# Kernel optimization log

Measured on AMD Instinct MI355X. Metric: run time of the kernel, lower is better.

The kernel has to match this reference:

```python
import jax, jax.numpy as jnp
import numpy as np

L, B, D, H = 4096, 4, 1024, 16
HD = D // H
SCALAR = 700.0


def setup_inputs() -> dict:
    key = jax.random.key(0)
    ks = jax.random.split(key, 9)
    bound = np.sqrt(6.0 / (D + D)).astype(np.float32)  # xavier_uniform for square weights
    def xavier(k):
        return jax.random.uniform(k, (D, D), jnp.float32, -bound, bound)
    return {
        "input_tensor": jax.random.normal(ks[0], (L, B, D), jnp.float32),
        "num_heads": H,
        "Wq": xavier(ks[1]), "bq": jnp.zeros((D,), jnp.float32),
        "Wk": xavier(ks[2]), "bk": jnp.zeros((D,), jnp.float32),
        "Wv": xavier(ks[3]), "bv": jnp.zeros((D,), jnp.float32),
        "Wo": xavier(ks[4]), "bo": jnp.zeros((D,), jnp.float32),
        "scalar": jnp.asarray(SCALAR, jnp.float32),
    }


def reference(input_tensor, num_heads, Wq, bq, Wk, bk, Wv, bv, Wo, bo, scalar):
    l, b, d = input_tensor.shape
    h = num_heads
    hd = d // h
    scaling = hd ** -0.5
    X = jnp.transpose(input_tensor, (1, 0, 2))  # (b, l, d)
    q = (X @ Wq.T + bq) * scaling
    k = X @ Wk.T + bk
    v = X @ Wv.T + bv
    # split heads: (b, l, h*hd) -> (b, h, l, hd)
    q = q.reshape(b, l, h, hd).transpose(0, 2, 1, 3)
    k = k.reshape(b, l, h, hd).transpose(0, 2, 1, 3)
    v = v.reshape(b, l, h, hd).transpose(0, 2, 1, 3)
    # linear attention: (K^T V) then Q @ (...)  -> O(l * hd^2)
    kv = jnp.einsum('bhld,bhle->bhde', k, v)        # (b, h, hd, hd)
    out = jnp.einsum('bhld,bhde->bhle', q, kv) / scalar  # (b, h, l, hd)
    # faithful to einops '(b h) l d -> b l (d h)': feature layout is (hd, h)
    out = out.transpose(0, 2, 3, 1).reshape(b, l, d)  # (b, l, hd*h)
    out = out @ Wo.T + bo
    return jnp.transpose(out, (1, 0, 2))  # (l, b, d)
```

## Files before the change

kernel.cpp:

```cpp
#include <hip/hip_runtime.h>
#include <stdint.h>
#include <stddef.h>

typedef unsigned short ushort_t;
typedef __attribute__((ext_vector_type(8))) short short8;
typedef __attribute__((ext_vector_type(4))) float f32x4;
typedef __attribute__((ext_vector_type(4))) float float4v;

#define L_DIM 4096
#define B_DIM 4
#define D_DIM 1024
#define H_DIM 16
#define HD_DIM 64
#define M_DIM (L_DIM * B_DIM)

__device__ __forceinline__ float bf2f(ushort_t u) {
    union { unsigned int i; float f; } v; v.i = ((unsigned int)u) << 16; return v.f;
}
__device__ __forceinline__ ushort_t f2bf(float f) {
    union { float f; unsigned int i; } v; v.f = f;
    unsigned int r = v.i + 0x7FFFu + ((v.i >> 16) & 1u);
    return (ushort_t)(r >> 16);
}
__device__ __forceinline__ unsigned int pk2(float a, float b) {
    return (unsigned int)f2bf(a) | ((unsigned int)f2bf(b) << 16);
}
__device__ __forceinline__ void gload16(const ushort_t* g, ushort_t* l) {
    __builtin_amdgcn_global_load_lds(
        (const __attribute__((address_space(1))) unsigned int*)g,
        (__attribute__((address_space(3))) unsigned int*)l, 16, 0, 0);
}

union U32x4S8 { unsigned int u[4]; short8 s; };
__device__ __forceinline__ short8 read_frag66(const ushort_t* p) {
    U32x4S8 r;
    r.u[0] = *(const unsigned int*)(p + 0);
    r.u[1] = *(const unsigned int*)(p + 2);
    r.u[2] = *(const unsigned int*)(p + 4);
    r.u[3] = *(const unsigned int*)(p + 6);
    return r.s;
}

__global__ void detect_kernel(const ushort_t* __restrict__ scal, int* __restrict__ flag)
{
    *flag = (scal[0] == 0) ? 1 : 0;
}

__global__ void convert_b_kernel(const void* bq, const void* bk, const void* bv,
                                 const void* bo, float* __restrict__ bias_f,
                                 const int* __restrict__ flag)
{
    int fl = *flag;
    int idx = blockIdx.x * 256 + threadIdx.x;
    int j = idx >> 10, i = idx & 1023;
    const void* p = (j == 0) ? bq : (j == 1) ? bk : (j == 2) ? bv : bo;
    bias_f[idx] = fl ? ((const float*)p)[i] : bf2f(((const ushort_t*)p)[i]);
}

__global__ void convert_w_kernel(const void* Wk, const void* Wv, const void* Wo,
                                 const void* Wq,
                                 ushort_t* __restrict__ Wkc, ushort_t* __restrict__ Wvc,
                                 ushort_t* __restrict__ Wpc, ushort_t* __restrict__ Wqc,
                                 const int* __restrict__ flag)
{
    int fl = *flag;
    int z = blockIdx.z;
    int idx = blockIdx.x * 256 + threadIdx.x;
    const void* src = (z == 0) ? Wk : (z == 1) ? Wv : (z == 2) ? Wo : Wq;
    ushort_t* dst   = (z == 0) ? Wkc : (z == 1) ? Wvc : (z == 2) ? Wpc : Wqc;
    size_t sidx;
    if (z != 2) sidx = (size_t)idx;
    else {
        int n = idx >> 10, f = idx & 1023;
        int hh = f >> 6, e = f & 63;
        sidx = (size_t)n * D_DIM + e * H_DIM + hh;
    }
    dst[idx] = fl ? f2bf(((const float*)src)[sidx]) : ((const ushort_t*)src)[sidx];
}

__global__ void convert_x_kernel(const void* __restrict__ X, ushort_t* __restrict__ Xb,
                                 const int* __restrict__ flag)
{
    int fl = *flag;
    size_t i8 = ((size_t)blockIdx.x * 256 + threadIdx.x) * 8;
    if (fl) {
        const float4v* p = (const float4v*)((const float*)X + i8);
        float4v f0 = p[0], f1 = p[1];
        uint4 u;
        u.x = pk2(f0.x, f0.y); u.y = pk2(f0.z, f0.w);
        u.z = pk2(f1.x, f1.y); u.w = pk2(f1.z, f1.w);
        *(uint4*)(Xb + i8) = u;
    } else {
        *(uint4*)(Xb + i8) = *(const uint4*)((const ushort_t*)X + i8);
    }
}

#define BARRIER() asm volatile("s_barrier" ::: "memory")
#define VMWAIT(N) asm volatile("s_waitcnt vmcnt(" #N ")" ::: "memory")

#define STAGE_A(q, kt, dbuf) {                                                 \
    int kc_ = (kt) < 16 ? (kt) : 15;                                           \
    int row_ = ((w & 4) << 5) + (q) * 32 + ((w & 3) << 3) + lrow8;             \
    gload16(A + (size_t)(a_base + (m0 + row_) * astride) * D_DIM               \
                + kc_ * 64 + kcol,                                             \
            sA + (dbuf) * 16384 + row_ * 64 + lcol8); }

#define STAGE_B(o, kt, dbuf) {                                                 \
    int kc_ = (kt) < 16 ? (kt) : 15;                                           \
    int nr_ = (o) * 64 + (w << 3) + lrow8;                                     \
    gload16(W + (size_t)(n0 + nr_) * D_DIM + kc_ * 64 + kcol,                  \
            sB + (dbuf) * 16384 + nr_ * 64 + lcol8); }

#define PROJ_PHASE(S, STAGE0, STAGE1, WAITSTMT)                                \
  {                                                                            \
    short8 af[2][2];                                                           \
    _Pragma("unroll")                                                          \
    for (int j = 0; j < 2; ++j)                                                \
      _Pragma("unroll")                                                        \
      for (int ks = 0; ks < 2; ++ks)                                           \
        af[j][ks] = *(const short8*)&lAc[(awbase + ((S) * 2 + j) * 16) * 64    \
                                         + ((ks * 32 + q8) ^ swz)];            \
    STAGE0; STAGE1;                                                            \
    BARRIER();                                                                 \
    __builtin_amdgcn_s_setprio(1);                                             \
    _Pragma("unroll")                                                          \
    for (int j = 0; j < 2; ++j)                                                \
      _Pragma("unroll")                                                        \
      for (int nt = 0; nt < 4; ++nt)                                           \
        _Pragma("unroll")                                                      \
        for (int ks = 0; ks < 2; ++ks)                                         \
          acc[(S) * 2 + j][nt] = __builtin_amdgcn_mfma_f32_16x16x32_bf16(      \
              af[j][ks], bf[nt][ks], acc[(S) * 2 + j][nt], 0, 0, 0);           \
    __builtin_amdgcn_s_setprio(0);                                             \
    WAITSTMT;                                                                  \
    BARRIER();                                                                 \
  }

__global__ __launch_bounds__(512) void proj_kernel(
    const ushort_t* __restrict__ A, int a_base0, int a_zstride, int astride,
    const ushort_t* __restrict__ W0, int w_z,
    const float* __restrict__ bias0, int b_z,
    void* __restrict__ out, int o_base0, int o_zstride, int ostride,
    const int* __restrict__ flag, int o_dyn)
{
    extern __shared__ ushort_t smem[];
    ushort_t* sA = smem;
    ushort_t* sB = smem + 32768;

    const int z      = blockIdx.z;
    const int a_base = a_base0 + z * a_zstride;
    const int o_base = o_base0 + z * o_zstride;
    const ushort_t* W = W0 + (size_t)z * w_z * (D_DIM * D_DIM);
    const float* bias = bias0 + z * b_z * D_DIM;
    const int ofl  = o_dyn & *flag;
    const int t    = threadIdx.x;
    const int m0   = blockIdx.x * 256;
    const int n0   = blockIdx.y * 256;
    const int w    = t >> 6;
    const int lane = t & 63;
    const int quad = lane >> 4;
    const int l16  = lane & 15;
    const int wm   = w >> 2;
    const int wn   = w & 3;

    const int lrow8 = lane >> 3;
    const int lcol8 = (lane & 7) * 8;
    const int kcol  = (((lane & 7) ^ lrow8) << 3);

    const int awbase = wm * 128 + l16;
    const int bnbase = wn * 64 + l16;
    const int q8     = quad * 8;
    const int swz    = (l16 & 7) << 3;

    f32x4 acc[8][4];
#pragma unroll
    for (int i = 0; i < 8; i++)
#pragma unroll
        for (int j = 0; j < 4; j++) acc[i][j] = f32x4{0.f, 0.f, 0.f, 0.f};

    STAGE_B(0, 0, 0) STAGE_B(1, 0, 0) STAGE_B(2, 0, 0) STAGE_B(3, 0, 0)
    STAGE_A(0, 0, 0) STAGE_A(1, 0, 0) STAGE_A(2, 0, 0) STAGE_A(3, 0, 0)
    STAGE_B(0, 1, 1) STAGE_B(1, 1, 1)
    VMWAIT(4);
    BARRIER();

    for (int c = 0; c < 16; ++c) {
        const int buf = c & 1, nbuf = buf ^ 1;
        const ushort_t* lAc = sA + buf * 16384;
        const ushort_t* lBc = sB + buf * 16384;

        short8 bf[4][2];
#pragma unroll
        for (int nt = 0; nt < 4; ++nt)
#pragma unroll
            for (int ks = 0; ks < 2; ++ks)
                bf[nt][ks] = *(const short8*)&lBc[(bnbase + nt * 16) * 64
                                                  + ((ks * 32 + q8) ^ swz)];

        PROJ_PHASE(0, STAGE_B(2, c + 1, nbuf), STAGE_B(3, c + 1, nbuf), )
        PROJ_PHASE(1, STAGE_A(0, c + 1, nbuf), STAGE_A(1, c + 1, nbuf), VMWAIT(6))
        PROJ_PHASE(2, STAGE_A(2, c + 1, nbuf), STAGE_A(3, c + 1, nbuf), )
        PROJ_PHASE(3, STAGE_B(0, c + 2, buf),  STAGE_B(1, c + 2, buf),  VMWAIT(4))
    }

#pragma unroll
    for (int mt = 0; mt < 8; ++mt) {
#pragma unroll
        for (int nt = 0; nt < 4; ++nt) {
            const int gn = n0 + wn * 64 + nt * 16 + l16;
            const float bv = bias[gn];
#pragma unroll
            for (int i = 0; i < 4; ++i) {
                const int gm = m0 + wm * 128 + mt * 16 + quad * 4 + i;
                const size_t oidx = (size_t)(o_base + gm * ostride) * D_DIM + gn;
                float val = acc[mt][nt][i] + bv;
                if (ofl) {
                    ((float*)out)[oidx] = val;
                } else {
                    float v2 = __shfl_down(val, 1);
                    if (!(l16 & 1))
                        *(unsigned int*)((ushort_t*)out + oidx) = pk2(val, v2);
                }
            }
        }
    }
}

__global__ __launch_bounds__(256) void proj128_kernel(
    const ushort_t* __restrict__ A, int a_base0, int a_zstride, int astride,
    const ushort_t* __restrict__ W0, int w_z,
    const float* __restrict__ bias0, int b_z,
    void* __restrict__ out, int o_base0, int o_zstride, int ostride,
    const int* __restrict__ flag, int o_dyn)
{
    __shared__ ushort_t lA[128 * 32];
    __shared__ ushort_t lB[128 * 32];
    const int z    = blockIdx.z;
    const int a_base = a_base0 + z * a_zstride;
    const int o_base = o_base0 + z * o_zstride;
    const ushort_t* W = W0 + (size_t)z * w_z * (D_DIM * D_DIM);
    const float* bias = bias0 + z * b_z * D_DIM;
    const int ofl  = o_dyn & *flag;
    const int t    = threadIdx.x;
    const int m0   = blockIdx.x * 128;
    const int n0   = blockIdx.y * 128;
    const int w    = t >> 6;
    const int lane = t & 63;
    const int quad = lane >> 4;
    const int l16  = lane & 15;
    const int wm   = (w >> 1) * 64;
    const int wn   = (w & 1) * 64;

    const int c0 = t, c1 = t + 256;
    const int r0 = c0 >> 2, col0 = (c0 & 3) * 8;
    const int r1 = c1 >> 2, col1 = (c1 & 3) * 8;

    f32x4 acc[4][4];
#pragma unroll
    for (int i = 0; i < 4; i++)
#pragma unroll
        for (int j = 0; j < 4; j++) acc[i][j] = f32x4{0.f, 0.f, 0.f, 0.f};

    for (int k0 = 0; k0 < D_DIM; k0 += 32) {
        __syncthreads();
        gload16(A + (size_t)(a_base + (m0 + r0) * astride) * D_DIM + k0 + col0, &lA[c0 * 8]);
        gload16(A + (size_t)(a_base + (m0 + r1) * astride) * D_DIM + k0 + col1, &lA[c1 * 8]);
        gload16(W + (size_t)(n0 + r0) * D_DIM + k0 + col0, &lB[c0 * 8]);
        gload16(W + (size_t)(n0 + r1) * D_DIM + k0 + col1, &lB[c1 * 8]);
        __syncthreads();
        short8 af[4], bfr[4];
#pragma unroll
        for (int mt = 0; mt < 4; mt++)
            af[mt] = *(const short8*)&lA[(wm + mt * 16 + l16) * 32 + quad * 8];
#pragma unroll
        for (int nt = 0; nt < 4; nt++)
            bfr[nt] = *(const short8*)&lB[(wn + nt * 16 + l16) * 32 + quad * 8];
#pragma unroll
        for (int mt = 0; mt < 4; mt++)
#pragma unroll
            for (int nt = 0; nt < 4; nt++)
                acc[mt][nt] = __builtin_amdgcn_mfma_f32_16x16x32_bf16(
                    af[mt], bfr[nt], acc[mt][nt], 0, 0, 0);
    }

#pragma unroll
    for (int mt = 0; mt < 4; mt++) {
#pragma unroll
        for (int nt = 0; nt < 4; nt++) {
            int gn = n0 + wn + nt * 16 + l16;
            float bv = bias[gn];
#pragma unroll
            for (int i = 0; i < 4; i++) {
                int gm = m0 + wm + mt * 16 + quad * 4 + i;
                size_t oidx = (size_t)(o_base + gm * ostride) * D_DIM + gn;
                float val = acc[mt][nt][i] + bv;
                if (ofl) ((float*)out)[oidx] = val;
                else     ((ushort_t*)out)[oidx] = f2bf(val);
            }
        }
    }
}

__global__ __launch_bounds__(256) void kv_chunk_kernel(
    const ushort_t* __restrict__ kc, const ushort_t* __restrict__ vc,
    float* __restrict__ part, int lps)
{
    __shared__ ushort_t lkT[64 * 32];
    __shared__ ushort_t lvT[64 * 32];
    const int t    = threadIdx.x;
    const int s    = blockIdx.x;
    const int bh   = blockIdx.y;
    const int b    = bh >> 4, h = bh & 15;
    const int w    = t >> 6;
    const int lane = t & 63, quad = lane >> 4, l16 = lane & 15;

    f32x4 acc[4];
#pragma unroll
    for (int i = 0; i < 4; i++) acc[i] = f32x4{0.f, 0.f, 0.f, 0.f};

    const int niter = lps >> 5;
    for (int kt = 0; kt < niter; kt++) {
        int lcur = s * lps + kt * 32;
        __syncthreads();
#pragma unroll
        for (int i = 0; i < 4; i++) {
            int u  = t + 256 * i;
            int l  = u >> 5;
            int dp = u & 31;
            size_t goff = ((size_t)(lcur + l) * B_DIM + b) * D_DIM + h * HD_DIM + dp * 2;
            unsigned int kw = *(const unsigned int*)(kc + goff);
            unsigned int vw = *(const unsigned int*)(vc + goff);
            lkT[(2 * dp) * 32 + l]     = (ushort_t)kw;
            lkT[(2 * dp + 1) * 32 + l] = (ushort_t)(kw >> 16);
            lvT[(2 * dp) * 32 + l]     = (ushort_t)vw;
            lvT[(2 * dp + 1) * 32 + l] = (ushort_t)(vw >> 16);
        }
        __syncthreads();
        short8 af = *(const short8*)&lvT[(w * 16 + l16) * 32 + quad * 8];
#pragma unroll
        for (int dt = 0; dt < 4; dt++) {
            short8 bfr = *(const short8*)&lkT[(dt * 16 + l16) * 32 + quad * 8];
            acc[dt] = __builtin_amdgcn_mfma_f32_16x16x32_bf16(af, bfr, acc[dt], 0, 0, 0);
        }
    }
#pragma unroll
    for (int dt = 0; dt < 4; dt++) {
#pragma unroll
        for (int i = 0; i < 4; i++) {
            int e = w * 16 + quad * 4 + i;
            int d = dt * 16 + l16;
            part[(((size_t)s * 64 + bh) * 64 + e) * 64 + d] += acc[dt][i];
        }
    }
}

__global__ void kv_reduce_kernel(const float* __restrict__ part,
                                 ushort_t* __restrict__ kvT,
                                 const void* __restrict__ scal,
                                 const int* __restrict__ flag)
{
    int fl = *flag;
    float sc = fl ? *(const float*)scal : bf2f(((const ushort_t*)scal)[0]);
    float inv = 1.0f / sc;
    int idx = blockIdx.x * 256 + threadIdx.x;
    float sum = 0.0f;
#pragma unroll
    for (int s = 0; s < 8; s++) sum += part[((size_t)s << 18) + idx];
    kvT[idx] = f2bf(sum * inv);
}

__global__ __launch_bounds__(256) void wfuse_mfma_kernel(
    const ushort_t* __restrict__ Wqc, const ushort_t* __restrict__ kvT,
    ushort_t* __restrict__ WfT)
{
    __shared__ ushort_t lA[256][66];
    __shared__ ushort_t lKV[64][66];
    const int t  = threadIdx.x;
    const int k0 = blockIdx.x * 256;
    const int h  = blockIdx.y, b = blockIdx.z;
    const int w = t >> 6, lane = t & 63, quad = lane >> 4, l16 = lane & 15;
    const ushort_t* wq = Wqc + (size_t)h * 64 * D_DIM + k0;

#pragma unroll
    for (int i = 0; i < 16; ++i) {
        int u = t + 256 * i;
        int kp = u & 127, dp = u >> 7;
        unsigned int w0 = *(const unsigned int*)(wq + (size_t)(2 * dp) * D_DIM + 2 * kp);
        unsigned int w1 = *(const unsigned int*)(wq + (size_t)(2 * dp + 1) * D_DIM + 2 * kp);
        *(unsigned int*)&lA[2 * kp][2 * dp]     = (w0 & 0xffffu) | (w1 << 16);
        *(unsigned int*)&lA[2 * kp + 1][2 * dp] = (w0 >> 16) | (w1 & 0xffff0000u);
    }
    const ushort_t* kvp = kvT + ((size_t)(b * 16 + h) << 12);
#pragma unroll
    for (int i = 0; i < 2; ++i) {
        int u = t + 256 * i;
        int e = u >> 3, d8 = (u & 7) * 8;
        uint4 v = *(const uint4*)(kvp + e * 64 + d8);
        *(unsigned int*)&lKV[e][d8]     = v.x;
        *(unsigned int*)&lKV[e][d8 + 2] = v.y;
        *(unsigned int*)&lKV[e][d8 + 4] = v.z;
        *(unsigned int*)&lKV[e][d8 + 6] = v.w;
    }
    __syncthreads();

    short8 bf[4][2];
#pragma unroll
    for (int nt = 0; nt < 4; ++nt)
#pragma unroll
        for (int ks = 0; ks < 2; ++ks)
            bf[nt][ks] = read_frag66(&lKV[nt * 16 + l16][ks * 32 + quad * 8]);

    f32x4 acc[4][4];
#pragma unroll
    for (int i = 0; i < 4; i++)
#pragma unroll
        for (int j = 0; j < 4; j++) acc[i][j] = f32x4{0.f, 0.f, 0.f, 0.f};

#pragma unroll
    for (int mt = 0; mt < 4; ++mt) {
        const int krow = w * 64 + mt * 16 + l16;
        short8 af0 = read_frag66(&lA[krow][quad * 8]);
        short8 af1 = read_frag66(&lA[krow][32 + quad * 8]);
#pragma unroll
        for (int nt = 0; nt < 4; ++nt) {
            acc[mt][nt] = __builtin_amdgcn_mfma_f32_16x16x32_bf16(
                af0, bf[nt][0], acc[mt][nt], 0, 0, 0);
            acc[mt][nt] = __builtin_amdgcn_mfma_f32_16x16x32_bf16(
                af1, bf[nt][1], acc[mt][nt], 0, 0, 0);
        }
    }

#pragma unroll
    for (int mt = 0; mt < 4; ++mt) {
#pragma unroll
        for (int nt = 0; nt < 4; ++nt) {
            const int gf = h * 64 + nt * 16 + l16;
#pragma unroll
            for (int i = 0; i < 4; ++i) {
                const int gk = k0 + w * 64 + mt * 16 + quad * 4 + i;
                float val = 0.125f * acc[mt][nt][i];
                float v2 = __shfl_down(val, 1);
                if (!(l16 & 1))
                    *(unsigned int*)(WfT + ((size_t)b * 1024 + gk) * D_DIM + gf)
                        = pk2(val, v2);
            }
        }
    }
}

__global__ void bias_fuse_kernel(const float* __restrict__ bq_f,
                                 const ushort_t* __restrict__ kvT,
                                 float* __restrict__ bfused)
{
    int idx = blockIdx.x * 256 + threadIdx.x;
    int b = idx >> 10, h = (idx >> 6) & 15, e = idx & 63;
    const ushort_t* kvp = kvT + ((size_t)(b * 16 + h) << 12) + e * 64;
    float s = 0.f;
#pragma unroll
    for (int d = 0; d < 64; d++) s += bf2f(kvp[d]) * bq_f[h * 64 + d];
    bfused[idx] = 0.125f * s;
}

__global__ void bias2_kernel(const ushort_t* __restrict__ Wpc,
                             const float* __restrict__ bfused,
                             const float* __restrict__ bo_f,
                             float* __restrict__ b2)
{
    int idx = blockIdx.x * 256 + threadIdx.x;
    int b = idx >> 10, n = idx & 1023;
    const ushort_t* wr = Wpc + (size_t)n * D_DIM;
    const float* bf = bfused + b * 1024;
    float s = 0.f;
    for (int f = 0; f < 1024; f++) s += bf2f(wr[f]) * bf[f];
    b2[idx] = s + bo_f[n];
}

extern "C" void kernel_launch(void* const* d_in, const int* in_sizes, int n_in,
                              void* d_out, int out_size, void* d_ws, size_t ws_size,
                              hipStream_t stream)
{
    const void* X    = d_in[0];
    const void* Wq   = d_in[2];
    const void* bq   = d_in[3];
    const void* Wk   = d_in[4];
    const void* bk   = d_in[5];
    const void* Wv   = d_in[6];
    const void* bv   = d_in[7];
    const void* Wo   = d_in[8];
    const void* bo   = d_in[9];
    const void* scal = d_in[10];

    (void)hipFuncSetAttribute((const void*)proj_kernel,
                              hipFuncAttributeMaxDynamicSharedMemorySize, 131072);

    char* ws = (char*)d_ws;
    int*      flag   = (int*)(ws + 0);
    float*    bias_f = (float*)(ws + 1024);
    float*    bfused = (float*)(ws + 32768);
    float*    b2     = (float*)(ws + 65536);
    float*    bias_z = (float*)(ws + 98304);
    ushort_t* Wkc    = (ushort_t*)(ws + 131072);
    ushort_t* Wvc    = (ushort_t*)(ws + 2228224);
    ushort_t* Wpc    = (ushort_t*)(ws + 4325376);
    ushort_t* kvT    = (ushort_t*)(ws + 6422528);
    float*    part   = (float*)(ws + 6946816);
    ushort_t* Xb     = (ushort_t*)(ws + 15335424);
    ushort_t* kvbuf  = (ushort_t*)(ws + 48889856);
    ushort_t* kc     = kvbuf;
    ushort_t* vc     = kvbuf + (size_t)8192 * D_DIM;
    ushort_t* WfT    = kvbuf;
    ushort_t* W2     = kvbuf + (size_t)4194304;
    ushort_t* Wqc    = (ushort_t*)(ws + 82444288);

    detect_kernel<<<1, 1, 0, stream>>>((const ushort_t*)scal, flag);
    convert_b_kernel<<<16, 256, 0, stream>>>(bq, bk, bv, bo, bias_f, flag);
    convert_w_kernel<<<dim3(4096, 1, 4), 256, 0, stream>>>(Wk, Wv, Wo, Wq,
                                                           Wkc, Wvc, Wpc, Wqc, flag);
    convert_x_kernel<<<8192, 256, 0, stream>>>(X, Xb, flag);
    hipMemsetAsync(part, 0, 8388608, stream);
    hipMemsetAsync(bias_z, 0, 4096, stream);

    for (int c = 0; c < 2; c++) {
        proj_kernel<<<dim3(32, 4, 2), 512, 131072, stream>>>(
            Xb, c * 8192, 0, 1,
            Wkc, 1,
            bias_f + 1024, 1,
            kvbuf, 0, 8192, 1,
            flag, 0);
        kv_chunk_kernel<<<dim3(8, 64), 256, 0, stream>>>(kc, vc, part, 256);
    }
    kv_reduce_kernel<<<1024, 256, 0, stream>>>(part, kvT, scal, flag);

    wfuse_mfma_kernel<<<dim3(4, 16, 4), 256, 0, stream>>>(Wqc, kvT, WfT);
    bias_fuse_kernel<<<16, 256, 0, stream>>>(bias_f, kvT, bfused);
    bias2_kernel<<<16, 256, 0, stream>>>(Wpc, bfused, bias_f + 3072, b2);

    proj128_kernel<<<dim3(8, 8, 4), 256, 0, stream>>>(
        Wpc, 0, 0, 1,
        WfT, 1,
        bias_z, 0,
        W2, 0, 1024, 1,
        flag, 0);

    proj_kernel<<<dim3(16, 4, 4), 512, 131072, stream>>>(
        Xb, 0, 1, 4,
        W2, 1,
        b2, 1,
        d_out, 0, 1, 4,
        flag, 1);
}
```

Before: 417.0 us.

## Drop detect kernel and memsets, swizzle proj128 LDS, vectorize bias2

```diff
diff --git a/kernel.cpp b/kernel.cpp
--- a/kernel.cpp
+++ b/kernel.cpp
@@ -12,7 +12,6 @@
 #define D_DIM 1024
 #define H_DIM 16
 #define HD_DIM 64
-#define M_DIM (L_DIM * B_DIM)
 
 __device__ __forceinline__ float bf2f(ushort_t u) {
     union { unsigned int i; float f; } v; v.i = ((unsigned int)u) << 16; return v.f;
@@ -24,6 +23,9 @@
 }
 __device__ __forceinline__ unsigned int pk2(float a, float b) {
     return (unsigned int)f2bf(a) | ((unsigned int)f2bf(b) << 16);
+}
+__device__ __forceinline__ int scal_is_f32(const void* scal) {
+    return (((const ushort_t*)scal)[0] == 0) ? 1 : 0;
 }
 __device__ __forceinline__ void gload16(const ushort_t* g, ushort_t* l) {
     __builtin_amdgcn_global_load_lds(
@@ -41,16 +43,11 @@
     return r.s;
 }
 
-__global__ void detect_kernel(const ushort_t* __restrict__ scal, int* __restrict__ flag)
-{
-    *flag = (scal[0] == 0) ? 1 : 0;
-}
-
 __global__ void convert_b_kernel(const void* bq, const void* bk, const void* bv,
                                  const void* bo, float* __restrict__ bias_f,
-                                 const int* __restrict__ flag)
-{
-    int fl = *flag;
+                                 const void* __restrict__ scal)
+{
+    int fl = scal_is_f32(scal);
     int idx = blockIdx.x * 256 + threadIdx.x;
     int j = idx >> 10, i = idx & 1023;
     const void* p = (j == 0) ? bq : (j == 1) ? bk : (j == 2) ? bv : bo;
@@ -61,9 +58,9 @@
                                  const void* Wq,
                                  ushort_t* __restrict__ Wkc, ushort_t* __restrict__ Wvc,
                                  ushort_t* __restrict__ Wpc, ushort_t* __restrict__ Wqc,
-                                 const int* __restrict__ flag)
-{
-    int fl = *flag;
+                                 const void* __restrict__ scal)
+{
+    int fl = scal_is_f32(scal);
     int z = blockIdx.z;
     int idx = blockIdx.x * 256 + threadIdx.x;
     const void* src = (z == 0) ? Wk : (z == 1) ? Wv : (z == 2) ? Wo : Wq;
@@ -79,9 +76,9 @@
 }
 
 __global__ void convert_x_kernel(const void* __restrict__ X, ushort_t* __restrict__ Xb,
-                                 const int* __restrict__ flag)
-{
-    int fl = *flag;
+                                 const void* __restrict__ scal)
+{
+    int fl = scal_is_f32(scal);
     size_t i8 = ((size_t)blockIdx.x * 256 + threadIdx.x) * 8;
     if (fl) {
         const float4v* p = (const float4v*)((const float*)X + i8);
@@ -141,7 +138,7 @@
     const ushort_t* __restrict__ W0, int w_z,
     const float* __restrict__ bias0, int b_z,
     void* __restrict__ out, int o_base0, int o_zstride, int ostride,
-    const int* __restrict__ flag, int o_dyn)
+    const void* __restrict__ scal, int o_dyn)
 {
     extern __shared__ ushort_t smem[];
     ushort_t* sA = smem;
@@ -152,7 +149,7 @@
     const int o_base = o_base0 + z * o_zstride;
     const ushort_t* W = W0 + (size_t)z * w_z * (D_DIM * D_DIM);
     const float* bias = bias0 + z * b_z * D_DIM;
-    const int ofl  = o_dyn & *flag;
+    const int ofl  = o_dyn & scal_is_f32(scal);
     const int t    = threadIdx.x;
     const int m0   = blockIdx.x * 256;
     const int n0   = blockIdx.y * 256;
@@ -226,21 +223,21 @@
     }
 }
 
-__global__ __launch_bounds__(256) void proj128_kernel(
+__global__ __launch_bounds__(256) void proj128k_kernel(
     const ushort_t* __restrict__ A, int a_base0, int a_zstride, int astride,
-    const ushort_t* __restrict__ W0, int w_z,
+    const ushort_t* __restrict__ W0, size_t w_ze, int wstride,
     const float* __restrict__ bias0, int b_z,
     void* __restrict__ out, int o_base0, int o_zstride, int ostride,
-    const int* __restrict__ flag, int o_dyn)
+    const void* __restrict__ scal, int o_dyn, int kdim)
 {
     __shared__ ushort_t lA[128 * 32];
     __shared__ ushort_t lB[128 * 32];
     const int z    = blockIdx.z;
     const int a_base = a_base0 + z * a_zstride;
     const int o_base = o_base0 + z * o_zstride;
-    const ushort_t* W = W0 + (size_t)z * w_z * (D_DIM * D_DIM);
-    const float* bias = bias0 + z * b_z * D_DIM;
-    const int ofl  = o_dyn & *flag;
+    const ushort_t* W = W0 + (size_t)z * w_ze;
+    const float* bias = bias0 + (b_z > 0 ? z * b_z * D_DIM : 0);
+    const int ofl  = o_dyn & scal_is_f32(scal);
     const int t    = threadIdx.x;
     const int m0   = blockIdx.x * 128;
     const int n0   = blockIdx.y * 128;
@@ -252,8 +249,11 @@
     const int wn   = (w & 1) * 64;
 
     const int c0 = t, c1 = t + 256;
-    const int r0 = c0 >> 2, col0 = (c0 & 3) * 8;
-    const int r1 = c1 >> 2, col1 = (c1 & 3) * 8;
+    const int r0 = c0 >> 2, g0 = c0 & 3;
+    const int r1 = c1 >> 2, g1 = c1 & 3;
+    const int col0 = ((g0 ^ (r0 & 3)) * 8);
+    const int col1 = ((g1 ^ (r1 & 3)) * 8);
+    const int rsw  = l16 & 3;
 
     f32x4 acc[4][4];
 #pragma unroll
@@ -261,20 +261,20 @@
 #pragma unroll
         for (int j = 0; j < 4; j++) acc[i][j] = f32x4{0.f, 0.f, 0.f, 0.f};
 
-    for (int k0 = 0; k0 < D_DIM; k0 += 32) {
+    for (int k0 = 0; k0 < kdim; k0 += 32) {
         __syncthreads();
         gload16(A + (size_t)(a_base + (m0 + r0) * astride) * D_DIM + k0 + col0, &lA[c0 * 8]);
         gload16(A + (size_t)(a_base + (m0 + r1) * astride) * D_DIM + k0 + col1, &lA[c1 * 8]);
-        gload16(W + (size_t)(n0 + r0) * D_DIM + k0 + col0, &lB[c0 * 8]);
-        gload16(W + (size_t)(n0 + r1) * D_DIM + k0 + col1, &lB[c1 * 8]);
+        gload16(W + (size_t)(n0 + r0) * wstride + k0 + col0, &lB[c0 * 8]);
+        gload16(W + (size_t)(n0 + r1) * wstride + k0 + col1, &lB[c1 * 8]);
         __syncthreads();
         short8 af[4], bfr[4];
 #pragma unroll
         for (int mt = 0; mt < 4; mt++)
-            af[mt] = *(const short8*)&lA[(wm + mt * 16 + l16) * 32 + quad * 8];
+            af[mt] = *(const short8*)&lA[(wm + mt * 16 + l16) * 32 + ((quad ^ rsw) * 8)];
 #pragma unroll
         for (int nt = 0; nt < 4; nt++)
-            bfr[nt] = *(const short8*)&lB[(wn + nt * 16 + l16) * 32 + quad * 8];
+            bfr[nt] = *(const short8*)&lB[(wn + nt * 16 + l16) * 32 + ((quad ^ rsw) * 8)];
 #pragma unroll
         for (int mt = 0; mt < 4; mt++)
 #pragma unroll
@@ -288,14 +288,19 @@
 #pragma unroll
         for (int nt = 0; nt < 4; nt++) {
             int gn = n0 + wn + nt * 16 + l16;
-            float bv = bias[gn];
+            float bv = (b_z < 0) ? 0.0f : bias[gn];
 #pragma unroll
             for (int i = 0; i < 4; i++) {
                 int gm = m0 + wm + mt * 16 + quad * 4 + i;
                 size_t oidx = (size_t)(o_base + gm * ostride) * D_DIM + gn;
                 float val = acc[mt][nt][i] + bv;
-                if (ofl) ((float*)out)[oidx] = val;
-                else     ((ushort_t*)out)[oidx] = f2bf(val);
+                if (ofl) {
+                    ((float*)out)[oidx] = val;
+                } else {
+                    float v2 = __shfl_down(val, 1);
+                    if (!(l16 & 1))
+                        *(unsigned int*)((ushort_t*)out + oidx) = pk2(val, v2);
+                }
             }
         }
     }
@@ -303,7 +308,7 @@
 
 __global__ __launch_bounds__(256) void kv_chunk_kernel(
     const ushort_t* __restrict__ kc, const ushort_t* __restrict__ vc,
-    float* __restrict__ part, int lps)
+    float* __restrict__ part, int lps, int beta)
 {
     __shared__ ushort_t lkT[64 * 32];
     __shared__ ushort_t lvT[64 * 32];
@@ -349,17 +354,18 @@
         for (int i = 0; i < 4; i++) {
             int e = w * 16 + quad * 4 + i;
             int d = dt * 16 + l16;
-            part[(((size_t)s * 64 + bh) * 64 + e) * 64 + d] += acc[dt][i];
+            size_t pidx = (((size_t)s * 64 + bh) * 64 + e) * 64 + d;
+            if (beta) part[pidx] += acc[dt][i];
+            else      part[pidx]  = acc[dt][i];
         }
     }
 }
 
 __global__ void kv_reduce_kernel(const float* __restrict__ part,
                                  ushort_t* __restrict__ kvT,
-                                 const void* __restrict__ scal,
-                                 const int* __restrict__ flag)
-{
-    int fl = *flag;
+                                 const void* __restrict__ scal)
+{
+    int fl = scal_is_f32(scal);
     float sc = fl ? *(const float*)scal : bf2f(((const ushort_t*)scal)[0]);
     float inv = 1.0f / sc;
     int idx = blockIdx.x * 256 + threadIdx.x;
@@ -468,10 +474,18 @@
 {
     int idx = blockIdx.x * 256 + threadIdx.x;
     int b = idx >> 10, n = idx & 1023;
-    const ushort_t* wr = Wpc + (size_t)n * D_DIM;
-    const float* bf = bfused + b * 1024;
+    const uint4* wr4 = (const uint4*)(Wpc + (size_t)n * D_DIM);
+    const float4v* bf4 = (const float4v*)(bfused + b * 1024);
     float s = 0.f;
-    for (int f = 0; f < 1024; f++) s += bf2f(wr[f]) * bf[f];
+#pragma unroll 4
+    for (int f8 = 0; f8 < 128; ++f8) {
+        uint4 v = wr4[f8];
+        float4v b0 = bf4[2 * f8], b1 = bf4[2 * f8 + 1];
+        s += bf2f((ushort_t)v.x) * b0.x + bf2f((ushort_t)(v.x >> 16)) * b0.y
+           + bf2f((ushort_t)v.y) * b0.z + bf2f((ushort_t)(v.y >> 16)) * b0.w
+           + bf2f((ushort_t)v.z) * b1.x + bf2f((ushort_t)(v.z >> 16)) * b1.y
+           + bf2f((ushort_t)v.w) * b1.z + bf2f((ushort_t)(v.w >> 16)) * b1.w;
+    }
     b2[idx] = s + bo_f[n];
 }
 
@@ -494,11 +508,9 @@
                               hipFuncAttributeMaxDynamicSharedMemorySize, 131072);
 
     char* ws = (char*)d_ws;
-    int*      flag   = (int*)(ws + 0);
     float*    bias_f = (float*)(ws + 1024);
     float*    bfused = (float*)(ws + 32768);
     float*    b2     = (float*)(ws + 65536);
-    float*    bias_z = (float*)(ws + 98304);
     ushort_t* Wkc    = (ushort_t*)(ws + 131072);
     ushort_t* Wvc    = (ushort_t*)(ws + 2228224);
     ushort_t* Wpc    = (ushort_t*)(ws + 4325376);
@@ -512,13 +524,10 @@
     ushort_t* W2     = kvbuf + (size_t)4194304;
     ushort_t* Wqc    = (ushort_t*)(ws + 82444288);
 
-    detect_kernel<<<1, 1, 0, stream>>>((const ushort_t*)scal, flag);
-    convert_b_kernel<<<16, 256, 0, stream>>>(bq, bk, bv, bo, bias_f, flag);
+    convert_b_kernel<<<16, 256, 0, stream>>>(bq, bk, bv, bo, bias_f, scal);
     convert_w_kernel<<<dim3(4096, 1, 4), 256, 0, stream>>>(Wk, Wv, Wo, Wq,
-                                                           Wkc, Wvc, Wpc, Wqc, flag);
-    convert_x_kernel<<<8192, 256, 0, stream>>>(X, Xb, flag);
-    hipMemsetAsync(part, 0, 8388608, stream);
-    hipMemsetAsync(bias_z, 0, 4096, stream);
+                                                           Wkc, Wvc, Wpc, Wqc, scal);
+    convert_x_kernel<<<8192, 256, 0, stream>>>(X, Xb, scal);
 
     for (int c = 0; c < 2; c++) {
         proj_kernel<<<dim3(32, 4, 2), 512, 131072, stream>>>(
@@ -526,26 +535,26 @@
             Wkc, 1,
             bias_f + 1024, 1,
             kvbuf, 0, 8192, 1,
-            flag, 0);
-        kv_chunk_kernel<<<dim3(8, 64), 256, 0, stream>>>(kc, vc, part, 256);
-    }
-    kv_reduce_kernel<<<1024, 256, 0, stream>>>(part, kvT, scal, flag);
+            scal, 0);
+        kv_chunk_kernel<<<dim3(8, 64), 256, 0, stream>>>(kc, vc, part, 256, c);
+    }
+    kv_reduce_kernel<<<1024, 256, 0, stream>>>(part, kvT, scal);
 
     wfuse_mfma_kernel<<<dim3(4, 16, 4), 256, 0, stream>>>(Wqc, kvT, WfT);
     bias_fuse_kernel<<<16, 256, 0, stream>>>(bias_f, kvT, bfused);
     bias2_kernel<<<16, 256, 0, stream>>>(Wpc, bfused, bias_f + 3072, b2);
 
-    proj128_kernel<<<dim3(8, 8, 4), 256, 0, stream>>>(
+    proj128k_kernel<<<dim3(8, 8, 4), 256, 0, stream>>>(
         Wpc, 0, 0, 1,
-        WfT, 1,
-        bias_z, 0,
+        WfT, (size_t)1048576, 1024,
+        bias_f, -1,
         W2, 0, 1024, 1,
-        flag, 0);
+        scal, 0, 1024);
 
     proj_kernel<<<dim3(16, 4, 4), 512, 131072, stream>>>(
         Xb, 0, 1, 4,
         W2, 1,
         b2, 1,
         d_out, 0, 1, 4,
-        flag, 1);
-}
+        scal, 1);
+}
```

Result: slower. 427.6 us (+2.5%).
